# Performance work log

Hardware: AMD Instinct MI355X
Metric: run time of the kernel (lower is better)

The kernel has to match this reference:

```python
import jax, jax.numpy as jnp
import numpy as np

N = 100_000      # nodes
E = 3_200_000    # edges (avg degree 32)
G = 512          # graphs in batch
IN_DIM = 3
H = 64
L = 3
BN_EPS = 1e-5


def setup_inputs() -> dict:
    key = jax.random.key(0)
    ks = jax.random.split(key, 14)
    s = 0.1
    x = jax.random.normal(ks[0], (N, IN_DIM), jnp.float32)
    edge_index = jax.random.randint(ks[1], (2, E), 0, N, dtype=jnp.int32)
    batch = jnp.sort(jax.random.randint(ks[2], (N,), 0, G, dtype=jnp.int32))
    # GIN MLP params per layer: Linear(in,H) -> ReLU -> Linear(H,H)
    w1_0 = jax.random.normal(ks[3], (IN_DIM, H), jnp.float32) * s   # layer 0 first linear
    w1_r = jax.random.normal(ks[4], (L - 1, H, H), jnp.float32) * s  # layers 1..L-1 first linear
    b1 = jax.random.normal(ks[5], (L, H), jnp.float32) * s
    w2 = jax.random.normal(ks[6], (L, H, H), jnp.float32) * s
    b2 = jax.random.normal(ks[7], (L, H), jnp.float32) * s
    gamma = 1.0 + jax.random.normal(ks[8], (L, H), jnp.float32) * 0.05
    beta = jax.random.normal(ks[9], (L, H), jnp.float32) * 0.05
    wout = jax.random.normal(ks[10], (H, H), jnp.float32) * s
    bout = jax.random.normal(ks[11], (H,), jnp.float32) * s
    return {"x": x, "edge_index": edge_index, "batch": batch,
            "w1_0": w1_0, "w1_r": w1_r, "b1": b1, "w2": w2, "b2": b2,
            "gamma": gamma, "beta": beta, "wout": wout, "bout": bout}


def reference(x, edge_index, batch, w1_0, w1_r, b1, w2, b2, gamma, beta, wout, bout):
    src, dst = edge_index[0], edge_index[1]
    for i in range(L):
        # GINConv: h = mlp((1+eps)*x + sum_{j in N(i)} x_j), eps = 0
        agg = jax.ops.segment_sum(x[src], dst, num_segments=N)  # [N, d]
        h = x + agg
        W1 = w1_0 if i == 0 else w1_r[i - 1]
        h = jax.nn.relu(h @ W1 + b1[i]) @ w2[i] + b2[i]          # [N, H]
        # BatchNorm1d (training mode: biased batch stats over nodes)
        mu = h.mean(axis=0)
        var = h.var(axis=0)
        h = (h - mu) / jnp.sqrt(var + BN_EPS) * gamma[i] + beta[i]
        x = jax.nn.relu(h)
    # global_mean_pool: segment mean over graph ids
    sums = jax.ops.segment_sum(x, batch, num_segments=G)                        # [G, H]
    cnt = jax.ops.segment_sum(jnp.ones((N, 1), x.dtype), batch, num_segments=G)  # [G, 1]
    graph_repr = jnp.where(cnt > 0, sums / jnp.maximum(cnt, 1.0), 0.0)
    return graph_repr @ wout + bout  # [G, H]
```

## Files before the change

kernel.cpp:

```cpp
#include <hip/hip_runtime.h>


#define NBMAX 1024
#define CAP 4608
#define CHUNK 8192
#define NBLK_MAX 512
#define MSTR 72

typedef __attribute__((ext_vector_type(8))) short bf16x8;
typedef __attribute__((ext_vector_type(4))) float f32x4;

static __device__ __forceinline__ bf16x8 as_bf16x8(uint4 u) {
    union { uint4 a; bf16x8 b; } x; x.a = u; return x.b;
}
static __device__ __forceinline__ unsigned short bf16r(float v) {
    unsigned u = __float_as_uint(v);
    return (unsigned short)((u + 0x7FFFu + ((u >> 16) & 1u)) >> 16);
}
static __device__ __forceinline__ unsigned bf16pack2(float a, float b) {
    return (unsigned)bf16r(a) | ((unsigned)bf16r(b) << 16);
}

__global__ void prep_weights(const float* __restrict__ w1_0, const float* __restrict__ w1_r,
                             const float* __restrict__ w2, unsigned short* __restrict__ w1T0,
                             unsigned short* __restrict__ w1T, unsigned short* __restrict__ w2T) {
    int t = blockIdx.x * 256 + threadIdx.x;
    if (t < 64 * 32) {
        int c = t >> 5, k = t & 31;
        w1T0[t] = bf16r(k < 3 ? w1_0[k * 64 + c] : 0.f);
    }
    if (t < 2 * 64 * 64) {
        int l = t >> 12, r = t & 4095, c = r >> 6, k = r & 63;
        w1T[t] = bf16r(w1_r[l * 4096 + k * 64 + c]);
    }
    if (t < 3 * 64 * 64) {
        int l = t >> 12, r = t & 4095, c = r >> 6, k = r & 63;
        w2T[t] = bf16r(w2[l * 4096 + k * 64 + c]);
    }
}

__global__ __launch_bounds__(512) void scatter_sort(
    const int* __restrict__ src, const int* __restrict__ dst,
    int* __restrict__ bucketed2, int* __restrict__ offsTab, int E) {
    __shared__ int hist[NBMAX];
    __shared__ int offs[NBMAX];
    __shared__ int stage[CHUNK];
    int t = threadIdx.x, blk = blockIdx.x;
    int e0 = blk * CHUNK, e1 = min(e0 + CHUNK, E);
    int len = e1 - e0;
    hist[t] = 0; hist[t + 512] = 0;
    __syncthreads();
    for (int e = e0 + t; e < e1; e += 512) atomicAdd(&hist[dst[e] >> 7], 1);
    __syncthreads();
    offs[t] = hist[t]; offs[t + 512] = hist[t + 512];
    __syncthreads();
    for (int off = 1; off < 1024; off <<= 1) {
        int v0 = (t >= off) ? offs[t - off] : 0;
        int v1 = offs[t + 512 - off];
        __syncthreads();
        offs[t] += v0;
        offs[t + 512] += v1;
        __syncthreads();
    }
    offs[t] -= hist[t]; offs[t + 512] -= hist[t + 512];
    hist[t] = 0; hist[t + 512] = 0;
    __syncthreads();
    offsTab[blk * 1025 + t] = offs[t];
    offsTab[blk * 1025 + t + 512] = offs[t + 512];
    if (t == 0) offsTab[blk * 1025 + 1024] = len;
    for (int e = e0 + t; e < e1; e += 512) {
        int d = dst[e];
        int bk = d >> 7;
        int r = offs[bk] + atomicAdd(&hist[bk], 1);
        stage[r] = src[e] | ((d & 127) << 20);
    }
    __syncthreads();
    for (int j = t; j < len; j += 512) bucketed2[e0 + j] = stage[j];
}

__global__ __launch_bounds__(256) void bucket_csr(
    const int* __restrict__ bucketed2, const int* __restrict__ offsTab,
    int* __restrict__ csrOut, int* __restrict__ rowstart, int* __restrict__ rowend,
    int N, int nblk) {
    __shared__ int ein[CAP];
    __shared__ int emid[CAP];
    __shared__ int runs[NBLK_MAX];
    __shared__ int rbeg[NBLK_MAX];
    __shared__ int hist[128];
    __shared__ int base[129];
    int b = blockIdx.x, t = threadIdx.x, node0 = b << 7;
    for (int r = t; r < NBLK_MAX; r += 256) {
        int l = 0, g0 = 0;
        if (r < nblk) {
            int beg = offsTab[r * 1025 + b];
            int end = offsTab[r * 1025 + b + 1];
            l = end - beg;
            g0 = r * CHUNK + beg;
        }
        runs[r] = l;
        rbeg[r] = g0;
    }
    __syncthreads();
    for (int off = 1; off < NBLK_MAX; off <<= 1) {
        int v0 = (t >= off) ? runs[t - off] : 0;
        int v1 = (t + 256 >= off) ? runs[t + 256 - off] : 0;
        __syncthreads();
        runs[t] += v0;
        runs[t + 256] += v1;
        __syncthreads();
    }
    int cnt = min(runs[NBLK_MAX - 1], CAP);
    for (int j = t; j < cnt; j += 256) {
        int lo = 0, hi = nblk - 1;
        while (lo < hi) {
            int m = (lo + hi) >> 1;
            if (runs[m] > j) hi = m; else lo = m + 1;
        }
        int st = lo ? runs[lo - 1] : 0;
        ein[j] = bucketed2[rbeg[lo] + (j - st)];
    }
    if (t < 128) hist[t] = 0;
    __syncthreads();
    for (int j = t; j < cnt; j += 256) atomicAdd(&hist[(ein[j] & 0xFFFFF) >> 10], 1);
    __syncthreads();
    if (t < 128) base[t + 1] = hist[t];
    if (t == 0) base[0] = 0;
    __syncthreads();
    for (int off = 1; off < 128; off <<= 1) {
        int v = 0;
        if (t < 128 && (t + 1) > off) v = base[t + 1 - off];
        __syncthreads();
        if (t < 128 && (t + 1) > off) base[t + 1] += v;
        __syncthreads();
    }
    if (t < 128) hist[t] = 0;
    __syncthreads();
    for (int j = t; j < cnt; j += 256) {
        int p = ein[j];
        int sb = (p & 0xFFFFF) >> 10;
        int pos = base[sb] + atomicAdd(&hist[sb], 1);
        emid[pos] = p;
    }
    __syncthreads();
    if (t < 128) hist[t] = 0;
    __syncthreads();
    for (int j = t; j < cnt; j += 256) atomicAdd(&hist[emid[j] >> 20], 1);
    __syncthreads();
    if (t < 128) base[t + 1] = hist[t];
    if (t == 0) base[0] = 0;
    __syncthreads();
    for (int off = 1; off < 128; off <<= 1) {
        int v = 0;
        if (t < 128 && (t + 1) > off) v = base[t + 1 - off];
        __syncthreads();
        if (t < 128 && (t + 1) > off) base[t + 1] += v;
        __syncthreads();
    }
    if (t < 128) {
        int n = node0 + t;
        if (n < N) {
            rowstart[n] = b * CAP + base[t];
            rowend[n] = b * CAP + base[t + 1];
        }
        hist[t] = 0;
    }
    __syncthreads();
    for (int j = t; j < cnt; j += 256) {
        int p = emid[j];
        int local = p >> 20;
        int pos = base[local] + atomicAdd(&hist[local], 1);
        ein[pos] = p & 0xFFFFF;
    }
    __syncthreads();
    for (int j = t; j < cnt; j += 256) csrOut[b * CAP + j] = ein[j];
}

__device__ __forceinline__ void accum_bf16(const uint4 u,
                                           const float4 scA, const float4 scB,
                                           const float4 shA, const float4 shB,
                                           float* __restrict__ a) {
    a[0] += fmaxf(__uint_as_float(u.x << 16) * scA.x + shA.x, 0.f);
    a[1] += fmaxf(__uint_as_float(u.x & 0xFFFF0000u) * scA.y + shA.y, 0.f);
    a[2] += fmaxf(__uint_as_float(u.y << 16) * scA.z + shA.z, 0.f);
    a[3] += fmaxf(__uint_as_float(u.y & 0xFFFF0000u) * scA.w + shA.w, 0.f);
    a[4] += fmaxf(__uint_as_float(u.z << 16) * scB.x + shB.x, 0.f);
    a[5] += fmaxf(__uint_as_float(u.z & 0xFFFF0000u) * scB.y + shB.y, 0.f);
    a[6] += fmaxf(__uint_as_float(u.w << 16) * scB.z + shB.z, 0.f);
    a[7] += fmaxf(__uint_as_float(u.w & 0xFFFF0000u) * scB.w + shB.w, 0.f);
}

template <bool L0>
__global__ __launch_bounds__(256) void gin_layer(
    const void* __restrict__ actInRaw,
    const int* __restrict__ rowstart, const int* __restrict__ rowend,
    const int* __restrict__ csr,
    const float* __restrict__ bnsumPrev, const float* __restrict__ bnsqPrev,
    const float* __restrict__ gammaPrev, const float* __restrict__ betaPrev,
    const uint4* __restrict__ w1Tu, const float* __restrict__ b1,
    const uint4* __restrict__ w2Tu, const float* __restrict__ b2,
    uint4* __restrict__ houtU4,
    float* __restrict__ partS, float* __restrict__ partQ, int N) {
    __shared__ __align__(16) unsigned short acts[32 * MSTR];
    __shared__ __align__(16) unsigned short mids[32 * MSTR];
    __shared__ float red[8][64];
    __shared__ float scs[64], shs[64];
    int t = threadIdx.x;
    int tileBase = blockIdx.x * 32;
    uint4* actsU4 = (uint4*)acts;
    const uint4* midU4 = (const uint4*)mids;
    const uint4 z4 = make_uint4(0, 0, 0, 0);

    if (!L0) {
        if (t < 64) {
            float mu = bnsumPrev[t] / (float)N;
            float var = bnsqPrev[t] / (float)N - mu * mu;
            float s = gammaPrev[t] * rsqrtf(var + 1e-5f);
            scs[t] = s;
            shs[t] = betaPrev[t] - mu * s;
        }
        __syncthreads();
    }

    {
        int ni = t >> 3, l = t & 7;
        int n = tileBase + ni;
        if (L0) {
            const float* x = (const float*)actInRaw;
            uint4 o = z4;
            if (l == 0 && n < N) {
                float s0 = x[n * 3], s1 = x[n * 3 + 1], s2 = x[n * 3 + 2];
                float b0 = 0.f, b1v = 0.f, b2v = 0.f;
                float c0 = 0.f, c1 = 0.f, c2 = 0.f;
                float d0 = 0.f, d1 = 0.f, d2 = 0.f;
                int s = rowstart[n], e = rowend[n];
                int j = s;
                for (; j + 3 < e; j += 4) {
                    int i0 = csr[j], i1 = csr[j + 1], i2 = csr[j + 2], i3 = csr[j + 3];
                    s0 += x[i0 * 3]; s1 += x[i0 * 3 + 1]; s2 += x[i0 * 3 + 2];
                    b0 += x[i1 * 3]; b1v += x[i1 * 3 + 1]; b2v += x[i1 * 3 + 2];
                    c0 += x[i2 * 3]; c1 += x[i2 * 3 + 1]; c2 += x[i2 * 3 + 2];
                    d0 += x[i3 * 3]; d1 += x[i3 * 3 + 1]; d2 += x[i3 * 3 + 2];
                }
                for (; j < e; j++) {
                    int nb = csr[j];
                    s0 += x[nb * 3]; s1 += x[nb * 3 + 1]; s2 += x[nb * 3 + 2];
                }
                s0 += b0 + c0 + d0; s1 += b1v + c1 + d1; s2 += b2v + c2 + d2;
                o = make_uint4(bf16pack2(s0, s1), bf16pack2(s2, 0.f), 0u, 0u);
            }
            actsU4[ni * 9 + l] = o;
        } else {
            const uint4* hr = (const uint4*)actInRaw;
            int c0i = l * 8;
            float4 scA = *(const float4*)&scs[c0i], scB = *(const float4*)&scs[c0i + 4];
            float4 shA = *(const float4*)&shs[c0i], shB = *(const float4*)&shs[c0i + 4];
            float A[8] = {0,0,0,0,0,0,0,0};
            float B[8] = {0,0,0,0,0,0,0,0};
            if (n < N) {
                accum_bf16(hr[(size_t)n * 8 + l], scA, scB, shA, shB, A);
                int s = rowstart[n], e = rowend[n];
                int j = s;
                for (; j + 3 < e; j += 4) {
                    int i0 = csr[j], i1 = csr[j + 1], i2 = csr[j + 2], i3 = csr[j + 3];
                    uint4 w0 = hr[(size_t)i0 * 8 + l];
                    uint4 w1 = hr[(size_t)i1 * 8 + l];
                    uint4 w2 = hr[(size_t)i2 * 8 + l];
                    uint4 w3 = hr[(size_t)i3 * 8 + l];
                    accum_bf16(w0, scA, scB, shA, shB, A);
                    accum_bf16(w1, scA, scB, shA, shB, B);
                    accum_bf16(w2, scA, scB, shA, shB, A);
                    accum_bf16(w3, scA, scB, shA, shB, B);
                }
                for (; j < e; j++) {
                    uint4 w = hr[(size_t)csr[j] * 8 + l];
                    accum_bf16(w, scA, scB, shA, shB, A);
                }
            }
            uint4 o;
            o.x = bf16pack2(A[0] + B[0], A[1] + B[1]);
            o.y = bf16pack2(A[2] + B[2], A[3] + B[3]);
            o.z = bf16pack2(A[4] + B[4], A[5] + B[5]);
            o.w = bf16pack2(A[6] + B[6], A[7] + B[7]);
            actsU4[ni * 9 + l] = o;
        }
    }

    int w = t >> 6, l64 = t & 63, m16 = l64 & 15, q = l64 >> 4;
    int col = w * 16 + m16;
    bf16x8 w1f0, w1f1, w2f0, w2f1;
    float bias1 = b1[col], bias2 = b2[col];
    if (L0) {
        w1f0 = as_bf16x8(w1Tu[col * 4 + q]);
    } else {
        w1f0 = as_bf16x8(w1Tu[col * 8 + q]);
        w1f1 = as_bf16x8(w1Tu[col * 8 + 4 + q]);
    }
    w2f0 = as_bf16x8(w2Tu[col * 8 + q]);
    w2f1 = as_bf16x8(w2Tu[col * 8 + 4 + q]);
    __syncthreads();
#pragma unroll
    for (int rg = 0; rg < 2; rg++) {
        int rloc = rg * 16 + m16;
        bf16x8 a0 = as_bf16x8(actsU4[rloc * 9 + q]);
        f32x4 acc = {bias1, bias1, bias1, bias1};
        if (L0) {
            acc = __builtin_amdgcn_mfma_f32_16x16x32_bf16(a0, w1f0, acc, 0, 0, 0);
        } else {
            bf16x8 a1 = as_bf16x8(actsU4[rloc * 9 + 4 + q]);
            acc = __builtin_amdgcn_mfma_f32_16x16x32_bf16(a0, w1f0, acc, 0, 0, 0);
            acc = __builtin_amdgcn_mfma_f32_16x16x32_bf16(a1, w1f1, acc, 0, 0, 0);
        }
#pragma unroll
        for (int r = 0; r < 4; r++) {
            int row = rg * 16 + q * 4 + r;
            mids[row * MSTR + col] = bf16r(fmaxf(acc[r], 0.f));
        }
    }
    __syncthreads();
    f32x4 accs[2];
#pragma unroll
    for (int rg = 0; rg < 2; rg++) {
        int rloc = rg * 16 + m16;
        bf16x8 a20 = as_bf16x8(midU4[rloc * 9 + q]);
        bf16x8 a21 = as_bf16x8(midU4[rloc * 9 + 4 + q]);
        f32x4 acc = {bias2, bias2, bias2, bias2};
        acc = __builtin_amdgcn_mfma_f32_16x16x32_bf16(a20, w2f0, acc, 0, 0, 0);
        acc = __builtin_amdgcn_mfma_f32_16x16x32_bf16(a21, w2f1, acc, 0, 0, 0);
        accs[rg] = acc;
    }
    float sA = 0.f, sB = 0.f, qA = 0.f, qB = 0.f;
#pragma unroll
    for (int rg = 0; rg < 2; rg++) {
#pragma unroll
        for (int r = 0; r < 4; r++) {
            int row = rg * 16 + q * 4 + r;
            float v = accs[rg][r];
            if (tileBase + row < N) {
                if (rg == 0) { sA += v; qA += v * v; } else { sB += v; qB += v * v; }
            }
            acts[row * MSTR + col] = bf16r(v);
        }
    }
    __syncthreads();
    {
        int row = t >> 3, qo = t & 7;
        int gr = tileBase + row;
        if (gr < N) houtU4[(size_t)gr * 8 + qo] = actsU4[row * 9 + qo];
    }
    red[q][col] = sA;
    red[4 + q][col] = sB;
    __syncthreads();
    if (t < 64) {
        float S = 0.f;
        for (int i = 0; i < 8; i++) S += red[i][t];
        partS[blockIdx.x * 64 + t] = S;
    }
    __syncthreads();
    red[q][col] = qA;
    red[4 + q][col] = qB;
    __syncthreads();
    if (t < 64) {
        float S = 0.f;
        for (int i = 0; i < 8; i++) S += red[i][t];
        partQ[blockIdx.x * 64 + t] = S;
    }
}

__global__ __launch_bounds__(256) void bn_reduce(
    const float* __restrict__ partS, const float* __restrict__ partQ,
    float* __restrict__ bnsum, float* __restrict__ bnsq, int nParts) {
    __shared__ float rs[256], rq[256];
    int b = blockIdx.x, t = threadIdx.x;
    float S = 0.f, Q = 0.f;
    for (int p = t; p < nParts; p += 256) {
        S += partS[p * 64 + b];
        Q += partQ[p * 64 + b];
    }
    rs[t] = S; rq[t] = Q;
    __syncthreads();
    for (int off = 128; off > 0; off >>= 1) {
        if (t < off) { rs[t] += rs[t + off]; rq[t] += rq[t + off]; }
        __syncthreads();
    }
    if (t == 0) { bnsum[b] = rs[0]; bnsq[b] = rq[0]; }
}

__device__ __forceinline__ int lowb(const int* __restrict__ a, int n, int v) {
    int lo = 0, hi = n;
    while (lo < hi) {
        int m = (lo + hi) >> 1;
        if (a[m] < v) lo = m + 1; else hi = m;
    }
    return lo;
}

__global__ __launch_bounds__(256) void bn_pool_out(
    const unsigned short* __restrict__ h, const int* __restrict__ batch,
    const float* __restrict__ bnsum, const float* __restrict__ bnsq,
    const float* __restrict__ gamma, const float* __restrict__ beta,
    const float* __restrict__ wout, const float* __restrict__ bout,
    float* __restrict__ out, int N) {
    __shared__ float sc[64], sh[64];
    __shared__ float part[4][64];
    __shared__ float gr[64];
    __shared__ int range[2];
    int g = blockIdx.x, t = threadIdx.x;
    if (t < 64) {
        float mu = bnsum[t] / (float)N;
        float var = bnsq[t] / (float)N - mu * mu;
        float s = gamma[t] * rsqrtf(var + 1e-5f);
        sc[t] = s;
        sh[t] = beta[t] - mu * s;
    }
    if (t == 64) range[0] = lowb(batch, N, g);
    if (t == 65) range[1] = lowb(batch, N, g + 1);
    __syncthreads();
    int s0 = range[0], s1 = range[1];
    int col = t & 63, ro = t >> 6;
    float acc = 0.f;
    for (int n = s0 + ro; n < s1; n += 4) {
        float v = __uint_as_float(((unsigned)h[(size_t)n * 64 + col]) << 16);
        acc += fmaxf(v * sc[col] + sh[col], 0.f);
    }
    part[ro][col] = acc;
    __syncthreads();
    if (t < 64) {
        float S = part[0][t] + part[1][t] + part[2][t] + part[3][t];
        float c = (float)(s1 - s0);
        gr[t] = (c > 0.f) ? S / c : 0.f;
    }
    __syncthreads();
    if (t < 64) {
        float a = bout[t];
        for (int f = 0; f < 64; f++) a += gr[f] * wout[f * 64 + t];
        out[g * 64 + t] = a;
    }
}

extern "C" void kernel_launch(void* const* d_in, const int* in_sizes, int n_in,
                              void* d_out, int out_size, void* d_ws, size_t ws_size,
                              hipStream_t stream) {
    const float* x     = (const float*)d_in[0];
    const int*   ei    = (const int*)d_in[1];
    const int*   batch = (const int*)d_in[2];
    const float* w1_0  = (const float*)d_in[3];
    const float* w1_r  = (const float*)d_in[4];
    const float* b1    = (const float*)d_in[5];
    const float* w2    = (const float*)d_in[6];
    const float* b2    = (const float*)d_in[7];
    const float* gamma = (const float*)d_in[8];
    const float* beta  = (const float*)d_in[9];
    const float* wout  = (const float*)d_in[10];
    const float* bout  = (const float*)d_in[11];
    float* out = (float*)d_out;

    const int N = in_sizes[2];
    const int E = in_sizes[1] / 2;
    const int NB = (N + 127) >> 7;
    const int nblk = (E + CHUNK - 1) / CHUNK;
    const int nT32 = (N + 31) >> 5;

    unsigned short* hbX = (unsigned short*)d_ws;
    unsigned short* hbY = hbX + (size_t)N * 64;
    int* bucketed2 = (int*)(hbY + (size_t)N * 64);
    int* offsTab   = bucketed2 + (size_t)nblk * CHUNK;
    int* csrOut    = offsTab + (size_t)nblk * 1025;
    int* rowstart  = csrOut + (size_t)NB * CAP;
    int* rowend    = rowstart + N;
    float* bnstats = (float*)(rowend + N);
    float* partS   = bnstats + 384;
    float* partQ   = partS + (size_t)nT32 * 64;
    unsigned short* w1T0 = (unsigned short*)(partQ + (size_t)nT32 * 64);
    unsigned short* w1T  = w1T0 + 64 * 32;
    unsigned short* w2T  = w1T + 2 * 64 * 64;

    const int* srcv = ei;
    const int* dstv = ei + E;

    prep_weights<<<48, 256, 0, stream>>>(w1_0, w1_r, w2, w1T0, w1T, w2T);

    scatter_sort<<<nblk, 512, 0, stream>>>(srcv, dstv, bucketed2, offsTab, E);
    bucket_csr<<<NB, 256, 0, stream>>>(bucketed2, offsTab, csrOut, rowstart, rowend, N, nblk);

    gin_layer<true><<<nT32, 256, 0, stream>>>(x, rowstart, rowend, csrOut,
                                              nullptr, nullptr, nullptr, nullptr,
                                              (const uint4*)w1T0, b1,
                                              (const uint4*)w2T, b2,
                                              (uint4*)hbX, partS, partQ, N);
    bn_reduce<<<64, 256, 0, stream>>>(partS, partQ, bnstats, bnstats + 64, nT32);

    gin_layer<false><<<nT32, 256, 0, stream>>>(hbX, rowstart, rowend, csrOut,
                                               bnstats, bnstats + 64, gamma, beta,
                                               (const uint4*)w1T, b1 + 64,
                                               (const uint4*)(w2T + 4096), b2 + 64,
                                               (uint4*)hbY, partS, partQ, N);
    bn_reduce<<<64, 256, 0, stream>>>(partS, partQ, bnstats + 128, bnstats + 192, nT32);

    gin_layer<false><<<nT32, 256, 0, stream>>>(hbY, rowstart, rowend, csrOut,
                                               bnstats + 128, bnstats + 192,
                                               gamma + 64, beta + 64,
                                               (const uint4*)(w1T + 4096), b1 + 128,
                                               (const uint4*)(w2T + 8192), b2 + 128,
                                               (uint4*)hbX, partS, partQ, N);
    bn_reduce<<<64, 256, 0, stream>>>(partS, partQ, bnstats + 256, bnstats + 320, nT32);

    bn_pool_out<<<512, 256, 0, stream>>>(hbX, batch, bnstats + 256, bnstats + 320,
                                         gamma + 128, beta + 128, wout, bout, out, N);
}
```

Before: 354.1 us.

## Use wavefront shuffle scans in CSR build and spread layer-0 gather across threads

Replaces the LDS Hillis-Steele prefix scans in scatter_sort and bucket_csr with wavefront __shfl_up scans plus a small cross-wave combine, cutting many __syncthreads barriers. The layer-0 aggregation, where previously only one of eight threads per node gathered neighbours, now splits each node's edge list across 8 segment threads and reduces partial sums through shared memory. Layer-0 MFMA input now zero-fills the unused quadrants instead of reading them from LDS. This adds an extra barrier and LDS staging in layer 0 and relies on mids being free to reuse as scratch.

```diff
diff --git a/kernel.cpp b/kernel.cpp
--- a/kernel.cpp
+++ b/kernel.cpp
@@ -45,6 +45,7 @@
     __shared__ int hist[NBMAX];
     __shared__ int offs[NBMAX];
     __shared__ int stage[CHUNK];
+    __shared__ int wsum8[8];
     int t = threadIdx.x, blk = blockIdx.x;
     int e0 = blk * CHUNK, e1 = min(e0 + CHUNK, E);
     int len = e1 - e0;
@@ -52,18 +53,23 @@
     __syncthreads();
     for (int e = e0 + t; e < e1; e += 512) atomicAdd(&hist[dst[e] >> 7], 1);
     __syncthreads();
-    offs[t] = hist[t]; offs[t + 512] = hist[t + 512];
-    __syncthreads();
-    for (int off = 1; off < 1024; off <<= 1) {
-        int v0 = (t >= off) ? offs[t - off] : 0;
-        int v1 = offs[t + 512 - off];
-        __syncthreads();
-        offs[t] += v0;
-        offs[t + 512] += v1;
-        __syncthreads();
-    }
-    offs[t] -= hist[t]; offs[t + 512] -= hist[t + 512];
-    hist[t] = 0; hist[t + 512] = 0;
+    int h0 = hist[2 * t], h1 = hist[2 * t + 1];
+    int pair = h0 + h1;
+    int lane = t & 63;
+    int incl = pair;
+#pragma unroll
+    for (int d = 1; d < 64; d <<= 1) {
+        int up = __shfl_up(incl, d);
+        if (lane >= d) incl += up;
+    }
+    if (lane == 63) wsum8[t >> 6] = incl;
+    __syncthreads();
+    int wid = t >> 6, wpre = 0;
+    for (int i = 0; i < wid; i++) wpre += wsum8[i];
+    int exclP = wpre + incl - pair;
+    offs[2 * t] = exclP;
+    offs[2 * t + 1] = exclP + h0;
+    hist[2 * t] = 0; hist[2 * t + 1] = 0;
     __syncthreads();
     offsTab[blk * 1025 + t] = offs[t];
     offsTab[blk * 1025 + t + 512] = offs[t + 512];
@@ -88,6 +94,8 @@
     __shared__ int rbeg[NBLK_MAX];
     __shared__ int hist[128];
     __shared__ int base[129];
+    __shared__ int wsum4[4];
+    __shared__ int wtot2[2];
     int b = blockIdx.x, t = threadIdx.x, node0 = b << 7;
     for (int r = t; r < NBLK_MAX; r += 256) {
         int l = 0, g0 = 0;
@@ -101,14 +109,25 @@
         rbeg[r] = g0;
     }
     __syncthreads();
-    for (int off = 1; off < NBLK_MAX; off <<= 1) {
-        int v0 = (t >= off) ? runs[t - off] : 0;
-        int v1 = (t + 256 >= off) ? runs[t + 256 - off] : 0;
+    {
+        int l0 = runs[2 * t], l1 = runs[2 * t + 1];
+        int pair = l0 + l1;
+        int lane = t & 63;
+        int incl = pair;
+#pragma unroll
+        for (int d = 1; d < 64; d <<= 1) {
+            int up = __shfl_up(incl, d);
+            if (lane >= d) incl += up;
+        }
+        if (lane == 63) wsum4[t >> 6] = incl;
         __syncthreads();
-        runs[t] += v0;
-        runs[t + 256] += v1;
-        __syncthreads();
-    }
+        int wid = t >> 6, wpre = 0;
+        for (int i = 0; i < wid; i++) wpre += wsum4[i];
+        int exclP = wpre + incl - pair;
+        runs[2 * t] = exclP + l0;
+        runs[2 * t + 1] = exclP + l0 + l1;
+    }
+    __syncthreads();
     int cnt = min(runs[NBLK_MAX - 1], CAP);
     for (int j = t; j < cnt; j += 256) {
         int lo = 0, hi = nblk - 1;
@@ -123,17 +142,21 @@
     __syncthreads();
     for (int j = t; j < cnt; j += 256) atomicAdd(&hist[(ein[j] & 0xFFFFF) >> 10], 1);
     __syncthreads();
-    if (t < 128) base[t + 1] = hist[t];
-    if (t == 0) base[0] = 0;
-    __syncthreads();
-    for (int off = 1; off < 128; off <<= 1) {
-        int v = 0;
-        if (t < 128 && (t + 1) > off) v = base[t + 1 - off];
+    {
+        int lane = t & 63;
+        int hv = (t < 128) ? hist[t] : 0;
+        int incl = hv;
+#pragma unroll
+        for (int d = 1; d < 64; d <<= 1) {
+            int up = __shfl_up(incl, d);
+            if (lane >= d) incl += up;
+        }
+        if (t < 128 && lane == 63) wtot2[t >> 6] = incl;
         __syncthreads();
-        if (t < 128 && (t + 1) > off) base[t + 1] += v;
-        __syncthreads();
-    }
-    if (t < 128) hist[t] = 0;
+        if (t >= 64 && t < 128) incl += wtot2[0];
+        if (t < 128) { base[t + 1] = incl; hist[t] = 0; }
+        if (t == 0) base[0] = 0;
+    }
     __syncthreads();
     for (int j = t; j < cnt; j += 256) {
         int p = ein[j];
@@ -146,23 +169,28 @@
     __syncthreads();
     for (int j = t; j < cnt; j += 256) atomicAdd(&hist[emid[j] >> 20], 1);
     __syncthreads();
-    if (t < 128) base[t + 1] = hist[t];
-    if (t == 0) base[0] = 0;
-    __syncthreads();
-    for (int off = 1; off < 128; off <<= 1) {
-        int v = 0;
-        if (t < 128 && (t + 1) > off) v = base[t + 1 - off];
+    {
+        int lane = t & 63;
+        int hv = (t < 128) ? hist[t] : 0;
+        int incl = hv;
+#pragma unroll
+        for (int d = 1; d < 64; d <<= 1) {
+            int up = __shfl_up(incl, d);
+            if (lane >= d) incl += up;
+        }
+        if (t < 128 && lane == 63) wtot2[t >> 6] = incl;
         __syncthreads();
-        if (t < 128 && (t + 1) > off) base[t + 1] += v;
-        __syncthreads();
-    }
+        if (t >= 64 && t < 128) incl += wtot2[0];
+        if (t < 128) { base[t + 1] = incl; hist[t] = 0; }
+        if (t == 0) base[0] = 0;
+    }
+    __syncthreads();
     if (t < 128) {
         int n = node0 + t;
         if (n < N) {
             rowstart[n] = b * CAP + base[t];
             rowend[n] = b * CAP + base[t + 1];
         }
-        hist[t] = 0;
     }
     __syncthreads();
     for (int j = t; j < cnt; j += 256) {
@@ -221,68 +249,69 @@
         __syncthreads();
     }
 
-    {
+    if (L0) {
+        const float* x = (const float*)actInRaw;
+        int ni = t & 31, seg = t >> 5;
+        int n = tileBase + ni;
+        float s0 = 0.f, s1 = 0.f, s2 = 0.f;
+        if (n < N) {
+            int srow = rowstart[n], erow = rowend[n];
+            for (int j = srow + seg; j < erow; j += 8) {
+                int nb = csr[j];
+                s0 += x[nb * 3]; s1 += x[nb * 3 + 1]; s2 += x[nb * 3 + 2];
+            }
+            if (seg == 0) { s0 += x[n * 3]; s1 += x[n * 3 + 1]; s2 += x[n * 3 + 2]; }
+        }
+        float* stg = (float*)mids;
+        stg[seg * 96 + ni * 3 + 0] = s0;
+        stg[seg * 96 + ni * 3 + 1] = s1;
+        stg[seg * 96 + ni * 3 + 2] = s2;
+        __syncthreads();
+        if (t < 32) {
+            float a0 = 0.f, a1 = 0.f, a2 = 0.f;
+#pragma unroll
+            for (int g2 = 0; g2 < 8; g2++) {
+                a0 += stg[g2 * 96 + t * 3 + 0];
+                a1 += stg[g2 * 96 + t * 3 + 1];
+                a2 += stg[g2 * 96 + t * 3 + 2];
+            }
+            actsU4[t * 9] = make_uint4(bf16pack2(a0, a1), bf16pack2(a2, 0.f), 0u, 0u);
+        }
+    } else {
+        const uint4* hr = (const uint4*)actInRaw;
         int ni = t >> 3, l = t & 7;
         int n = tileBase + ni;
-        if (L0) {
-            const float* x = (const float*)actInRaw;
-            uint4 o = z4;
-            if (l == 0 && n < N) {
-                float s0 = x[n * 3], s1 = x[n * 3 + 1], s2 = x[n * 3 + 2];
-                float b0 = 0.f, b1v = 0.f, b2v = 0.f;
-                float c0 = 0.f, c1 = 0.f, c2 = 0.f;
-                float d0 = 0.f, d1 = 0.f, d2 = 0.f;
-                int s = rowstart[n], e = rowend[n];
-                int j = s;
-                for (; j + 3 < e; j += 4) {
-                    int i0 = csr[j], i1 = csr[j + 1], i2 = csr[j + 2], i3 = csr[j + 3];
-                    s0 += x[i0 * 3]; s1 += x[i0 * 3 + 1]; s2 += x[i0 * 3 + 2];
-                    b0 += x[i1 * 3]; b1v += x[i1 * 3 + 1]; b2v += x[i1 * 3 + 2];
-                    c0 += x[i2 * 3]; c1 += x[i2 * 3 + 1]; c2 += x[i2 * 3 + 2];
-                    d0 += x[i3 * 3]; d1 += x[i3 * 3 + 1]; d2 += x[i3 * 3 + 2];
-                }
-                for (; j < e; j++) {
-                    int nb = csr[j];
-                    s0 += x[nb * 3]; s1 += x[nb * 3 + 1]; s2 += x[nb * 3 + 2];
-                }
-                s0 += b0 + c0 + d0; s1 += b1v + c1 + d1; s2 += b2v + c2 + d2;
-                o = make_uint4(bf16pack2(s0, s1), bf16pack2(s2, 0.f), 0u, 0u);
+        int c0i = l * 8;
+        float4 scA = *(const float4*)&scs[c0i], scB = *(const float4*)&scs[c0i + 4];
+        float4 shA = *(const float4*)&shs[c0i], shB = *(const float4*)&shs[c0i + 4];
+        float A[8] = {0,0,0,0,0,0,0,0};
+        float B[8] = {0,0,0,0,0,0,0,0};
+        if (n < N) {
+            accum_bf16(hr[(size_t)n * 8 + l], scA, scB, shA, shB, A);
+            int s = rowstart[n], e = rowend[n];
+            int j = s;
+            for (; j + 3 < e; j += 4) {
+                int i0 = csr[j], i1 = csr[j + 1], i2 = csr[j + 2], i3 = csr[j + 3];
+                uint4 w0 = hr[(size_t)i0 * 8 + l];
+                uint4 w1 = hr[(size_t)i1 * 8 + l];
+                uint4 w2 = hr[(size_t)i2 * 8 + l];
+                uint4 w3 = hr[(size_t)i3 * 8 + l];
+                accum_bf16(w0, scA, scB, shA, shB, A);
+                accum_bf16(w1, scA, scB, shA, shB, B);
+                accum_bf16(w2, scA, scB, shA, shB, A);
+                accum_bf16(w3, scA, scB, shA, shB, B);
             }
-            actsU4[ni * 9 + l] = o;
-        } else {
-            const uint4* hr = (const uint4*)actInRaw;
-            int c0i = l * 8;
-            float4 scA = *(const float4*)&scs[c0i], scB = *(const float4*)&scs[c0i + 4];
-            float4 shA = *(const float4*)&shs[c0i], shB = *(const float4*)&shs[c0i + 4];
-            float A[8] = {0,0,0,0,0,0,0,0};
-            float B[8] = {0,0,0,0,0,0,0,0};
-            if (n < N) {
-                accum_bf16(hr[(size_t)n * 8 + l], scA, scB, shA, shB, A);
-                int s = rowstart[n], e = rowend[n];
-                int j = s;
-                for (; j + 3 < e; j += 4) {
-                    int i0 = csr[j], i1 = csr[j + 1], i2 = csr[j + 2], i3 = csr[j + 3];
-                    uint4 w0 = hr[(size_t)i0 * 8 + l];
-                    uint4 w1 = hr[(size_t)i1 * 8 + l];
-                    uint4 w2 = hr[(size_t)i2 * 8 + l];
-                    uint4 w3 = hr[(size_t)i3 * 8 + l];
-                    accum_bf16(w0, scA, scB, shA, shB, A);
-                    accum_bf16(w1, scA, scB, shA, shB, B);
-                    accum_bf16(w2, scA, scB, shA, shB, A);
-                    accum_bf16(w3, scA, scB, shA, shB, B);
-                }
-                for (; j < e; j++) {
-                    uint4 w = hr[(size_t)csr[j] * 8 + l];
-                    accum_bf16(w, scA, scB, shA, shB, A);
-                }
+            for (; j < e; j++) {
+                uint4 w = hr[(size_t)csr[j] * 8 + l];
+                accum_bf16(w, scA, scB, shA, shB, A);
             }
-            uint4 o;
-            o.x = bf16pack2(A[0] + B[0], A[1] + B[1]);
-            o.y = bf16pack2(A[2] + B[2], A[3] + B[3]);
-            o.z = bf16pack2(A[4] + B[4], A[5] + B[5]);
-            o.w = bf16pack2(A[6] + B[6], A[7] + B[7]);
-            actsU4[ni * 9 + l] = o;
-        }
+        }
+        uint4 o;
+        o.x = bf16pack2(A[0] + B[0], A[1] + B[1]);
+        o.y = bf16pack2(A[2] + B[2], A[3] + B[3]);
+        o.z = bf16pack2(A[4] + B[4], A[5] + B[5]);
+        o.w = bf16pack2(A[6] + B[6], A[7] + B[7]);
+        actsU4[ni * 9 + l] = o;
     }
 
     int w = t >> 6, l64 = t & 63, m16 = l64 & 15, q = l64 >> 4;
@@ -301,7 +330,8 @@
 #pragma unroll
     for (int rg = 0; rg < 2; rg++) {
         int rloc = rg * 16 + m16;
-        bf16x8 a0 = as_bf16x8(actsU4[rloc * 9 + q]);
+        bf16x8 a0 = as_bf16x8(L0 ? (q == 0 ? actsU4[rloc * 9] : z4)
+                                 : actsU4[rloc * 9 + q]);
         f32x4 acc = {bias1, bias1, bias1, bias1};
         if (L0) {
             acc = __builtin_amdgcn_mfma_f32_16x16x32_bf16(a0, w1f0, acc, 0, 0, 0);
```

After: 345.4 us. -2.4%, faster.
